# Kernel optimization log

Hardware: AMD Instinct MI355X
Metric: run time of the kernel (lower is better)

## Reference

```python
import jax, jax.numpy as jnp
import numpy as np

N = 100000      # nodes
E = 1600000     # edges (avg degree 16)
NFEAT = 128
NHID = 128
NOUT = 1
BN_EPS = 1e-5


def setup_inputs() -> dict:
    key = jax.random.key(0)
    ks = jax.random.split(key, 8)
    s = 0.05  # weight scale for numerical stability through relu stack
    return {
        "x": jax.random.normal(ks[0], (N, NFEAT), jnp.float32),
        "edge_index": jax.random.randint(ks[1], (2, E), 0, N, dtype=jnp.int64),
        "edge_weight": jax.random.uniform(ks[2], (E,), jnp.float32),
        "conv1_W": jax.random.normal(ks[3], (NFEAT, NHID), jnp.float32) * s,
        "conv1_b": jnp.zeros((NHID,), jnp.float32),
        "conv2_W": jax.random.normal(ks[4], (NHID, NHID), jnp.float32) * s,
        "conv2_b": jnp.zeros((NHID,), jnp.float32),
        "bn1_gamma": jnp.ones((NHID,), jnp.float32),
        "bn1_beta": jnp.zeros((NHID,), jnp.float32),
        "bn2_gamma": jnp.ones((NHID,), jnp.float32),
        "bn2_beta": jnp.zeros((NHID,), jnp.float32),
        "fc1_W": jax.random.normal(ks[5], (NFEAT + 2 * NHID, NHID), jnp.float32) * s,
        "fc1_b": jnp.zeros((NHID,), jnp.float32),
        "fc2_W": jax.random.normal(ks[6], (NHID, NOUT), jnp.float32) * s,
        "fc2_b": jnp.zeros((NOUT,), jnp.float32),
    }


def _gcn_norm(edge_index, edge_weight, num_nodes):
    # PyG gcn_norm: add self-loops (weight 1), symmetric D^-1/2 A D^-1/2.
    row, col = edge_index[0], edge_index[1]
    loop = jnp.arange(num_nodes, dtype=row.dtype)
    rows = jnp.concatenate([row, loop])
    cols = jnp.concatenate([col, loop])
    w = jnp.concatenate([edge_weight, jnp.ones((num_nodes,), edge_weight.dtype)])
    deg = jax.ops.segment_sum(w, cols, num_segments=num_nodes)
    dinv = jnp.where(deg > 0, jax.lax.rsqrt(deg), 0.0)
    norm = dinv[rows] * w * dinv[cols]
    return rows, cols, norm


def _gcn_conv(x, rows, cols, norm, W, b, num_nodes):
    h = x @ W                                  # [N, out]
    msg = h[rows] * norm[:, None]              # gather + scale  [E+N, out]
    out = jax.ops.segment_sum(msg, cols, num_segments=num_nodes)  # scatter-add
    return out + b


def _bn(x, gamma, beta):
    # BatchNorm1d, training-mode batch statistics (biased variance)
    m = jnp.mean(x, axis=0)
    v = jnp.var(x, axis=0)
    return (x - m) * jax.lax.rsqrt(v + BN_EPS) * gamma + beta


def reference(x, edge_index, edge_weight, conv1_W, conv1_b, conv2_W, conv2_b,
              bn1_gamma, bn1_beta, bn2_gamma, bn2_beta,
              fc1_W, fc1_b, fc2_W, fc2_b):
    n = x.shape[0]
    rows, cols, norm = _gcn_norm(edge_index, edge_weight, n)
    h0 = x
    h1 = jax.nn.relu(_gcn_conv(h0, rows, cols, norm, conv1_W, conv1_b, n))
    h1 = _bn(h1, bn1_gamma, bn1_beta)          # dropout p=0 -> identity
    h2 = jax.nn.relu(_gcn_conv(h1, rows, cols, norm, conv2_W, conv2_b, n))
    h2 = _bn(h2, bn2_gamma, bn2_beta)
    cat = jnp.concatenate([h0, h1, h2], axis=1)   # [N, nfeat+2*nhid]
    z = jax.nn.relu(cat @ fc1_W + fc1_b)
    z = jax.nn.relu(z @ fc2_W + fc2_b)
    return z.reshape(-1)
```

## Files before the change

### kernel.cpp

```cpp
#include <hip/hip_runtime.h>

typedef __attribute__((ext_vector_type(8))) short short8;
typedef __attribute__((ext_vector_type(4))) float f32x4;

constexpr int N = 100000;
constexpr int E = 1600000;
constexpr int F = 128;
constexpr float EPS = 1e-5f;
constexpr int NB = (N + 1023) / 1024;

constexpr int R_RNG = 16;
constexpr int BINS = 6250;
constexpr int G2 = 64;
constexpr int NPB = 640;
constexpr int EPB = E / NPB;
constexpr int EPB4 = EPB / 4;

__device__ __forceinline__ short bf16hi(float v) {
  unsigned u = __float_as_uint(v);
  unsigned r = (u + 0x7fffu + ((u >> 16) & 1u)) >> 16;
  return (short)r;
}
__device__ __forceinline__ float bf16f(short h) {
  return __uint_as_float(((unsigned)(unsigned short)h) << 16);
}
__device__ __forceinline__ float bflo(unsigned v) {
  return __uint_as_float(v << 16);
}
__device__ __forceinline__ float bfhi(unsigned v) {
  return __uint_as_float(v & 0xffff0000u);
}

__global__ __launch_bounds__(256) void k_phist(const int* __restrict__ ei, int* __restrict__ Psl) {
  __shared__ int h16[16];
  const int b = blockIdx.x;
  const int tid = threadIdx.x;
  if (tid < 16) h16[tid] = 0;
  __syncthreads();
  const int4* cols4 = (const int4*)(ei + E);
  for (int t = tid; t < EPB4; t += 256) {
    int4 c = cols4[b * EPB4 + t];
    atomicAdd(&h16[c.x / BINS], 1);
    atomicAdd(&h16[c.y / BINS], 1);
    atomicAdd(&h16[c.z / BINS], 1);
    atomicAdd(&h16[c.w / BINS], 1);
  }
  __syncthreads();
  if (tid == 0) {
    int run = 0;
#pragma unroll
    for (int r = 0; r < 16; ++r) { Psl[b * 17 + r] = run; run += h16[r]; }
    Psl[b * 17 + 16] = run;
  }
}

__global__ __launch_bounds__(256) void k_pscatter(const int* __restrict__ ei, const float* __restrict__ ew,
                                                  const int* __restrict__ Psl, int2* __restrict__ pe) {
  __shared__ int cur[16];
  const int b = blockIdx.x;
  const int tid = threadIdx.x;
  if (tid < 16) cur[tid] = Psl[b * 17 + tid];
  __syncthreads();
  const int4* cols4 = (const int4*)(ei + E);
  const int4* rows4 = (const int4*)ei;
  const float4* ew4 = (const float4*)ew;
  const int base = b * EPB;
  for (int t = tid; t < EPB4; t += 256) {
    int4 c = cols4[b * EPB4 + t];
    int4 rr = rows4[b * EPB4 + t];
    float4 w = ew4[b * EPB4 + t];
#pragma unroll
    for (int j = 0; j < 4; ++j) {
      int cc = (j == 0) ? c.x : (j == 1) ? c.y : (j == 2) ? c.z : c.w;
      int rv = (j == 0) ? rr.x : (j == 1) ? rr.y : (j == 2) ? rr.z : rr.w;
      float wv = (j == 0) ? w.x : (j == 1) ? w.y : (j == 2) ? w.z : w.w;
      int r = cc / BINS;
      int pos = base + atomicAdd(&cur[r], 1);
      pe[pos] = make_int2((rv << 13) | (cc - r * BINS), __float_as_int(wv));
    }
  }
}

__global__ __launch_bounds__(256) void k_hist2(const int2* __restrict__ pe, const int* __restrict__ Psl,
                                               int* __restrict__ P) {
  __shared__ int hist[BINS];
  const int r = blockIdx.x / G2;
  const int g = blockIdx.x % G2;
  const int tid = threadIdx.x;
  for (int i = tid; i < BINS; i += 256) hist[i] = 0;
  __syncthreads();
  for (int b = g; b < NPB; b += G2) {
    const int s = Psl[b * 17 + r], e2 = Psl[b * 17 + r + 1];
    const int eb = b * EPB;
    for (int t = s + tid; t < e2; t += 256)
      atomicAdd(&hist[pe[eb + t].x & 0x1FFF], 1);
  }
  __syncthreads();
  for (int i = tid; i < BINS; i += 256) P[(size_t)blockIdx.x * BINS + i] = hist[i];
}

__global__ __launch_bounds__(256) void k_reduce(int* __restrict__ P, int* __restrict__ cnt) {
  int b = blockIdx.x * 256 + threadIdx.x;
  if (b >= N) return;
  int r = b / BINS, lb = b % BINS;
  size_t base = (size_t)r * G2 * BINS + lb;
  int run = 0;
#pragma unroll 4
  for (int g = 0; g < G2; ++g) {
    size_t idx = base + (size_t)g * BINS;
    int v = P[idx];
    P[idx] = run;
    run += v;
  }
  cnt[b] = run;
}

__global__ __launch_bounds__(256) void k_bsum(const int* __restrict__ cnt, int* __restrict__ bsum) {
  __shared__ int sh[256];
  int base = blockIdx.x * 1024 + threadIdx.x * 4;
  int s = 0;
  if (base + 3 < N) {
    int4 v = *(const int4*)&cnt[base];
    s = v.x + v.y + v.z + v.w;
  } else {
#pragma unroll
    for (int j = 0; j < 4; ++j)
      if (base + j < N) s += cnt[base + j];
  }
  sh[threadIdx.x] = s;
  __syncthreads();
  for (int o = 128; o > 0; o >>= 1) {
    if (threadIdx.x < o) sh[threadIdx.x] += sh[threadIdx.x + o];
    __syncthreads();
  }
  if (threadIdx.x == 0) bsum[blockIdx.x] = sh[0];
}

__global__ __launch_bounds__(128) void k_bscan(const int* __restrict__ bsum, int* __restrict__ bbase,
                                               int* __restrict__ offN) {
  __shared__ int sh[128];
  const int t = threadIdx.x;
  int v = (t < NB) ? bsum[t] : 0;
  sh[t] = v;
  __syncthreads();
  for (int o = 1; o < 128; o <<= 1) {
    int u = (t >= o) ? sh[t - o] : 0;
    __syncthreads();
    sh[t] += u;
    __syncthreads();
  }
  if (t < NB) bbase[t] = sh[t] - v;
  if (t == 127) *offN = sh[127];
}

__global__ __launch_bounds__(256) void k_off(const int* __restrict__ cnt, const int* __restrict__ bbase,
                                             int* __restrict__ off) {
  __shared__ int sh[256];
  int base = blockIdx.x * 1024 + threadIdx.x * 4;
  int c[4] = {0, 0, 0, 0};
  if (base + 3 < N) {
    int4 v = *(const int4*)&cnt[base];
    c[0] = v.x; c[1] = v.y; c[2] = v.z; c[3] = v.w;
  } else {
#pragma unroll
    for (int j = 0; j < 4; ++j)
      if (base + j < N) c[j] = cnt[base + j];
  }
  int s = c[0] + c[1] + c[2] + c[3];
  sh[threadIdx.x] = s;
  __syncthreads();
  for (int o = 1; o < 256; o <<= 1) {
    int u = (threadIdx.x >= o) ? sh[threadIdx.x - o] : 0;
    __syncthreads();
    sh[threadIdx.x] += u;
    __syncthreads();
  }
  int run = bbase[blockIdx.x] + sh[threadIdx.x] - s;
#pragma unroll
  for (int j = 0; j < 4; ++j) {
    if (base + j < N) { off[base + j] = run; run += c[j]; }
  }
}

__global__ __launch_bounds__(256) void k_scatter3(const int2* __restrict__ pe, const int* __restrict__ Psl,
                                                  const int* __restrict__ off, const int* __restrict__ P,
                                                  int2* __restrict__ cpair) {
  __shared__ int base[BINS];
  const int r = blockIdx.x / G2;
  const int g = blockIdx.x % G2;
  const int tid = threadIdx.x;
  for (int i = tid; i < BINS; i += 256)
    base[i] = off[r * BINS + i] + P[(size_t)blockIdx.x * BINS + i];
  __syncthreads();
  for (int b = g; b < NPB; b += G2) {
    const int s = Psl[b * 17 + r], e2 = Psl[b * 17 + r + 1];
    const int eb = b * EPB;
    for (int t = s + tid; t < e2; t += 256) {
      int2 p = pe[eb + t];
      int pos = atomicAdd(&base[p.x & 0x1FFF], 1);
      cpair[pos] = make_int2((int)(((unsigned)p.x) >> 13), p.y);
    }
  }
}

__global__ __launch_bounds__(256) void k_degcsc(const int2* __restrict__ cpair, const int* __restrict__ off,
                                                float* __restrict__ dinv) {
  int i = blockIdx.x * 256 + threadIdx.x;
  if (i >= N) return;
  int b = off[i], e2 = off[i + 1];
  float s = 1.0f;
  for (int p = b; p < e2; ++p) s += __int_as_float(cpair[p].y);
  dinv[i] = rsqrtf(s);
}

__global__ __launch_bounds__(256) void k_nrm(const int* __restrict__ off,
                                             const float* __restrict__ dinv, int2* __restrict__ cpair) {
  int i = blockIdx.x * 256 + threadIdx.x;
  if (i >= N) return;
  int b = off[i], e2 = off[i + 1];
  float di = dinv[i];
  for (int p = b; p < e2; ++p) {
    int2 cp = cpair[p];
    cpair[p].y = __float_as_int(dinv[cp.x] * __int_as_float(cp.y) * di);
  }
}

__global__ __launch_bounds__(256) void k_wprep_all(
    const float* __restrict__ W1, const float* __restrict__ W2, const float* __restrict__ Wf1,
    short* __restrict__ wt1h, short* __restrict__ wt1l,
    short* __restrict__ wt2h, short* __restrict__ wt2l,
    short* __restrict__ wtfh, short* __restrict__ wtfl,
    float* __restrict__ st1, float* __restrict__ st2) {
  int idx = blockIdx.x * 256 + threadIdx.x;
  if (idx < 256) st1[idx] = 0.f;
  else if (idx < 512) st2[idx - 256] = 0.f;
  const float* W;
  short *wh, *wl;
  int K, li;
  if (idx < 16384)      { W = W1;  wh = wt1h; wl = wt1l; K = 128; li = idx; }
  else if (idx < 32768) { W = W2;  wh = wt2h; wl = wt2l; K = 128; li = idx - 16384; }
  else if (idx < 81920) { W = Wf1; wh = wtfh; wl = wtfl; K = 384; li = idx - 32768; }
  else return;
  int k = li >> 7, c = li & 127;
  float v = W[(size_t)k * 128 + c];
  short h = bf16hi(v);
  short l = bf16hi(v - bf16f(h));
  wh[(size_t)c * K + k] = h;
  wl[(size_t)c * K + k] = l;
}

__global__ void k_bnparam(const float* __restrict__ st, const float* __restrict__ gamma,
                          const float* __restrict__ beta, float* __restrict__ p) {
  int t = threadIdx.x;
  if (t >= 128) return;
  const float inv_n = 1.0f / (float)N;
  float m = st[t] * inv_n;
  float var = fmaf(-m, m, st[128 + t] * inv_n);
  float sc = gamma[t] * rsqrtf(var + EPS);
  p[t] = sc;
  p[128 + t] = fmaf(-m, sc, beta[t]);
}

template <int KSTEPS, bool OBF16, bool FC2, int AMASK>
__global__ __launch_bounds__(256) void k_gemm_mfma(
    const void* __restrict__ a0, const float* __restrict__ p0,
    const void* __restrict__ a1, const float* __restrict__ p1,
    const void* __restrict__ a2, const float* __restrict__ p2,
    const short* __restrict__ wth, const short* __restrict__ wtl,
    const float* __restrict__ bias, void* __restrict__ Cout,
    const float* __restrict__ wf2, const float* __restrict__ bf2) {
  constexpr int KT = KSTEPS * 32;
  __shared__ short Ah[128][40];
  __shared__ short Al[128][40];
  __shared__ short Bh[128][40];
  __shared__ short Bl[128][40];
  __shared__ float red[2][128];

  const int tid = threadIdx.x;
  const int m0 = blockIdx.x * 128;
  const int sr = tid >> 1;
  const int sk = (tid & 1) * 16;
  const int arow = min(m0 + sr, N - 1);
  const int lane = tid & 63;
  const int lr = lane & 15;
  const int lg = lane >> 4;
  const int wv = tid >> 6;
  const int wr = wv >> 1;
  const int wc = wv & 1;

  f32x4 acc[4][4];
#pragma unroll
  for (int m = 0; m < 4; ++m)
#pragma unroll
    for (int n = 0; n < 4; ++n) acc[m][n] = (f32x4){0.f, 0.f, 0.f, 0.f};

  for (int ks = 0; ks < KSTEPS; ++ks) {
    const int seg = ks >> 2;
    const int koff = (ks & 3) * 32;
    const void* __restrict__ Av = (seg == 0) ? a0 : ((seg == 1) ? a1 : a2);
    const float* __restrict__ P = (seg == 0) ? p0 : ((seg == 1) ? p1 : p2);
    const bool isbf = (AMASK >> seg) & 1;

    float v[16];
    if (isbf) {
      const unsigned short* A16 = (const unsigned short*)Av;
      const uint4* s16 = (const uint4*)&A16[(size_t)arow * F + koff + sk];
      uint4 ua = s16[0], ub = s16[1];
      unsigned uu[8] = {ua.x, ua.y, ua.z, ua.w, ub.x, ub.y, ub.z, ub.w};
#pragma unroll
      for (int j = 0; j < 8; ++j) {
        v[2 * j] = bflo(uu[j]);
        v[2 * j + 1] = bfhi(uu[j]);
      }
    } else {
      const float* A = (const float*)Av;
      const float4* src = (const float4*)(A + (size_t)arow * F + koff + sk);
#pragma unroll
      for (int q = 0; q < 4; ++q) {
        float4 t = src[q];
        v[q * 4 + 0] = t.x; v[q * 4 + 1] = t.y; v[q * 4 + 2] = t.z; v[q * 4 + 3] = t.w;
      }
    }
    if (P) {
      const int c0 = koff + sk;
#pragma unroll
      for (int q = 0; q < 4; ++q) {
        float4 s = *(const float4*)&P[c0 + q * 4];
        float4 b = *(const float4*)&P[128 + c0 + q * 4];
        v[q * 4 + 0] = fmaf(v[q * 4 + 0], s.x, b.x);
        v[q * 4 + 1] = fmaf(v[q * 4 + 1], s.y, b.y);
        v[q * 4 + 2] = fmaf(v[q * 4 + 2], s.z, b.z);
        v[q * 4 + 3] = fmaf(v[q * 4 + 3], s.w, b.w);
      }
    }
    short hh[16], ll[16];
#pragma unroll
    for (int j = 0; j < 16; ++j) {
      hh[j] = bf16hi(v[j]);
      ll[j] = bf16hi(v[j] - bf16f(hh[j]));
    }

    __syncthreads();

    short8 t0, t1, u0, u1;
#pragma unroll
    for (int j = 0; j < 8; ++j) { t0[j] = hh[j]; t1[j] = hh[8 + j]; u0[j] = ll[j]; u1[j] = ll[8 + j]; }
    *(short8*)&Ah[sr][sk] = t0;
    *(short8*)&Ah[sr][sk + 8] = t1;
    *(short8*)&Al[sr][sk] = u0;
    *(short8*)&Al[sr][sk + 8] = u1;

    const size_t wbase = (size_t)sr * KT + ks * 32 + sk;
    *(short8*)&Bh[sr][sk]     = *(const short8*)&wth[wbase];
    *(short8*)&Bh[sr][sk + 8] = *(const short8*)&wth[wbase + 8];
    *(short8*)&Bl[sr][sk]     = *(const short8*)&wtl[wbase];
    *(short8*)&Bl[sr][sk + 8] = *(const short8*)&wtl[wbase + 8];

    __syncthreads();

    short8 afh[4], afl[4], bfh[4], bfl[4];
#pragma unroll
    for (int m = 0; m < 4; ++m) {
      const int r2 = wr * 64 + m * 16 + lr;
      afh[m] = *(const short8*)&Ah[r2][lg * 8];
      afl[m] = *(const short8*)&Al[r2][lg * 8];
    }
#pragma unroll
    for (int n = 0; n < 4; ++n) {
      const int c2 = wc * 64 + n * 16 + lr;
      bfh[n] = *(const short8*)&Bh[c2][lg * 8];
      bfl[n] = *(const short8*)&Bl[c2][lg * 8];
    }
#pragma unroll
    for (int m = 0; m < 4; ++m)
#pragma unroll
      for (int n = 0; n < 4; ++n) {
        acc[m][n] = __builtin_amdgcn_mfma_f32_16x16x32_bf16(afh[m], bfh[n], acc[m][n], 0, 0, 0);
        acc[m][n] = __builtin_amdgcn_mfma_f32_16x16x32_bf16(afl[m], bfh[n], acc[m][n], 0, 0, 0);
        acc[m][n] = __builtin_amdgcn_mfma_f32_16x16x32_bf16(afh[m], bfl[n], acc[m][n], 0, 0, 0);
      }
  }

  float bv[4];
#pragma unroll
  for (int n = 0; n < 4; ++n) bv[n] = bias ? bias[wc * 64 + n * 16 + lr] : 0.f;

  if (FC2) {
    float w2v[4];
#pragma unroll
    for (int n = 0; n < 4; ++n) w2v[n] = wf2[wc * 64 + n * 16 + lr];
#pragma unroll
    for (int m = 0; m < 4; ++m) {
#pragma unroll
      for (int j = 0; j < 4; ++j) {
        float partial = 0.f;
#pragma unroll
        for (int n = 0; n < 4; ++n)
          partial += fmaxf(acc[m][n][j] + bv[n], 0.f) * w2v[n];
#pragma unroll
        for (int o = 8; o >= 1; o >>= 1) partial += __shfl_xor(partial, o, 16);
        if (lr == 0) red[wc][wr * 64 + m * 16 + lg * 4 + j] = partial;
      }
    }
    __syncthreads();
    if (tid < 128) {
      const int row = m0 + tid;
      if (row < N) {
        float s = red[0][tid] + red[1][tid] + bf2[0];
        ((float*)Cout)[row] = fmaxf(s, 0.f);
      }
    }
  } else {
#pragma unroll
    for (int m = 0; m < 4; ++m) {
#pragma unroll
      for (int j = 0; j < 4; ++j) {
        const int row = m0 + wr * 64 + m * 16 + lg * 4 + j;
        if (row < N) {
#pragma unroll
          for (int n = 0; n < 4; ++n) {
            const int col = wc * 64 + n * 16 + lr;
            float o = acc[m][n][j] + bv[n];
            if (bias) o = fmaxf(o, 0.f);
            if (OBF16) {
              ((unsigned short*)Cout)[(size_t)row * F + col] = (unsigned short)bf16hi(o);
            } else {
              ((float*)Cout)[(size_t)row * F + col] = o;
            }
          }
        }
      }
    }
  }
}

__global__ __launch_bounds__(256) void k_agg(
    const unsigned* __restrict__ h,
    const int2* __restrict__ cpair, const int* __restrict__ off,
    const float* __restrict__ dinv, const float* __restrict__ bias,
    unsigned* __restrict__ out) {
  const int i = blockIdx.x * 4 + (threadIdx.x >> 6);
  if (i >= N) return;
  const int lane = threadIdx.x & 63;
  const float di = dinv[i];
  unsigned sv = h[(size_t)i * 64 + lane];
  float acc0 = di * di * bflo(sv);
  float acc1 = di * di * bfhi(sv);
  int e = off[i];
  const int eend = off[i + 1];
  for (; e + 8 <= eend; e += 8) {
    int2 cp[8];
    unsigned vv[8];
#pragma unroll
    for (int j = 0; j < 8; ++j) cp[j] = cpair[e + j];
#pragma unroll
    for (int j = 0; j < 8; ++j) vv[j] = h[(size_t)cp[j].x * 64 + lane];
#pragma unroll
    for (int j = 0; j < 8; ++j) {
      float w = __int_as_float(cp[j].y);
      acc0 = fmaf(w, bflo(vv[j]), acc0);
      acc1 = fmaf(w, bfhi(vv[j]), acc1);
    }
  }
  for (; e < eend; ++e) {
    int2 cp = cpair[e];
    float w = __int_as_float(cp.y);
    unsigned v = h[(size_t)cp.x * 64 + lane];
    acc0 = fmaf(w, bflo(v), acc0);
    acc1 = fmaf(w, bfhi(v), acc1);
  }
  float2 b = *(const float2*)&bias[lane * 2];
  float o0 = fmaxf(acc0 + b.x, 0.f);
  float o1 = fmaxf(acc1 + b.y, 0.f);
  unsigned pack = ((unsigned)(unsigned short)bf16hi(o0)) |
                  (((unsigned)(unsigned short)bf16hi(o1)) << 16);
  out[(size_t)i * 64 + lane] = pack;
}

__global__ __launch_bounds__(256) void k_stats(const unsigned* __restrict__ h2, float* __restrict__ sums) {
  const int cp = threadIdx.x & 63;
  const int q = threadIdx.x >> 6;
  float s0 = 0.f, s1 = 0.f, q0 = 0.f, q1 = 0.f;
  for (int r = blockIdx.x * 4 + q; r < N; r += gridDim.x * 4) {
    unsigned u = h2[(size_t)r * 64 + cp];
    float lo = bflo(u), hi = bfhi(u);
    s0 += lo; s1 += hi;
    q0 = fmaf(lo, lo, q0);
    q1 = fmaf(hi, hi, q1);
  }
  __shared__ float2 sh[256];
  sh[threadIdx.x] = make_float2(s0, s1);
  __syncthreads();
  if (q == 0) {
    float2 a = sh[cp], b = sh[64 + cp], c = sh[128 + cp], d = sh[192 + cp];
    atomicAdd(&sums[2 * cp], a.x + b.x + c.x + d.x);
    atomicAdd(&sums[2 * cp + 1], a.y + b.y + c.y + d.y);
  }
  __syncthreads();
  sh[threadIdx.x] = make_float2(q0, q1);
  __syncthreads();
  if (q == 0) {
    float2 a = sh[cp], b = sh[64 + cp], c = sh[128 + cp], d = sh[192 + cp];
    atomicAdd(&sums[128 + 2 * cp], a.x + b.x + c.x + d.x);
    atomicAdd(&sums[128 + 2 * cp + 1], a.y + b.y + c.y + d.y);
  }
}

extern "C" void kernel_launch(void* const* d_in, const int* in_sizes, int n_in,
                              void* d_out, int out_size, void* d_ws, size_t ws_size,
                              hipStream_t stream) {
  const float* x   = (const float*)d_in[0];
  const int*   ei  = (const int*)d_in[1];
  const float* ew  = (const float*)d_in[2];
  const float* W1  = (const float*)d_in[3];
  const float* b1  = (const float*)d_in[4];
  const float* W2  = (const float*)d_in[5];
  const float* b2  = (const float*)d_in[6];
  const float* g1  = (const float*)d_in[7];
  const float* be1 = (const float*)d_in[8];
  const float* g2  = (const float*)d_in[9];
  const float* be2 = (const float*)d_in[10];
  const float* Wf1 = (const float*)d_in[11];
  const float* bf1 = (const float*)d_in[12];
  const float* Wf2 = (const float*)d_in[13];
  const float* bf2 = (const float*)d_in[14];
  float* out = (float*)d_out;

  char* p = (char*)d_ws;
  auto take = [&](size_t bytes) {
    char* r = p;
    p += (bytes + 255) & ~(size_t)255;
    return r;
  };
  float* st1  = (float*)take(256 * 4);
  float* st2  = (float*)take(256 * 4);
  int*   cnt  = (int*)take((size_t)N * 4);
  int*   off  = (int*)take((size_t)(N + 1) * 4);
  int*   bsum = (int*)take((size_t)NB * 4);
  int*   bbase= (int*)take((size_t)NB * 4);
  int*   Psl  = (int*)take((size_t)NPB * 17 * 4);
  int2*  pe   = (int2*)take((size_t)E * 8);
  int*   Phist= (int*)take((size_t)R_RNG * G2 * BINS * 4);
  float* dinv = (float*)take((size_t)N * 4);
  float* p1   = (float*)take(256 * 4);
  float* p2   = (float*)take(256 * 4);
  short* wt1h = (short*)take((size_t)128 * 128 * 2);
  short* wt1l = (short*)take((size_t)128 * 128 * 2);
  short* wt2h = (short*)take((size_t)128 * 128 * 2);
  short* wt2l = (short*)take((size_t)128 * 128 * 2);
  short* wtfh = (short*)take((size_t)128 * 384 * 2);
  short* wtfl = (short*)take((size_t)128 * 384 * 2);
  int2*  cpair= (int2*)take((size_t)E * 8);
  unsigned short* bufH  = (unsigned short*)take((size_t)N * F * 2);
  unsigned short* bufB16= (unsigned short*)take((size_t)N * F * 2);
  unsigned short* bufC16= (unsigned short*)take((size_t)N * F * 2);

  k_wprep_all<<<320, 256, 0, stream>>>(W1, W2, Wf1, wt1h, wt1l, wt2h, wt2l, wtfh, wtfl, st1, st2);

  k_phist<<<NPB, 256, 0, stream>>>(ei, Psl);
  k_pscatter<<<NPB, 256, 0, stream>>>(ei, ew, Psl, pe);
  k_hist2<<<R_RNG * G2, 256, 0, stream>>>(pe, Psl, Phist);
  k_reduce<<<(N + 255) / 256, 256, 0, stream>>>(Phist, cnt);
  k_bsum<<<NB, 256, 0, stream>>>(cnt, bsum);
  k_bscan<<<1, 128, 0, stream>>>(bsum, bbase, &off[N]);
  k_off<<<NB, 256, 0, stream>>>(cnt, bbase, off);
  k_scatter3<<<R_RNG * G2, 256, 0, stream>>>(pe, Psl, off, Phist, cpair);
  k_degcsc<<<(N + 255) / 256, 256, 0, stream>>>(cpair, off, dinv);
  k_nrm<<<(N + 255) / 256, 256, 0, stream>>>(off, dinv, cpair);

  const int gemm_grid = (N + 127) / 128;
  k_gemm_mfma<4, true, false, 0><<<gemm_grid, 256, 0, stream>>>(
      x, nullptr, nullptr, nullptr, nullptr, nullptr, wt1h, wt1l, nullptr, bufH, nullptr, nullptr);
  k_agg<<<(N + 3) / 4, 256, 0, stream>>>((const unsigned*)bufH, cpair, off, dinv, b1,
                                         (unsigned*)bufB16);
  k_stats<<<256, 256, 0, stream>>>((const unsigned*)bufB16, st1);
  k_bnparam<<<1, 128, 0, stream>>>(st1, g1, be1, p1);
  k_gemm_mfma<4, true, false, 1><<<gemm_grid, 256, 0, stream>>>(
      bufB16, p1, nullptr, nullptr, nullptr, nullptr, wt2h, wt2l, nullptr, bufH, nullptr, nullptr);
  k_agg<<<(N + 3) / 4, 256, 0, stream>>>((const unsigned*)bufH, cpair, off, dinv, b2,
                                         (unsigned*)bufC16);
  k_stats<<<256, 256, 0, stream>>>((const unsigned*)bufC16, st2);
  k_bnparam<<<1, 128, 0, stream>>>(st2, g2, be2, p2);
  k_gemm_mfma<12, false, true, 6><<<gemm_grid, 256, 0, stream>>>(
      x, nullptr, bufB16, p1, bufC16, p2, wtfh, wtfl, bf1, out, Wf2, bf2);
}
```

Measured before the change: 442.3 us.

## Pack edge index and bf16 weight into 32 bits and split aggregation by feature half per XCD

The normalization kernel now writes a compact 4-byte edge record: a 17-bit source index and a 15-bit bf16 weight with the sign bit dropped, valid because weights are non-negative. The aggregation kernel reads these records instead of 8-byte int2 pairs, halving edge-list traffic. Each node is now handled by two blocks, one per 64-column feature half, with block ids mapped so each XCD group works on one half of the features, aiming for better L2 locality of the gathered rows. The costs are bf16 rounding of the edge weights, 2-byte gathers instead of 4-byte ones, and the edge list being read twice per node.

```diff
diff --git a/kernel.cpp b/kernel.cpp
--- a/kernel.cpp
+++ b/kernel.cpp
@@ -214,14 +214,18 @@
 }
 
 __global__ __launch_bounds__(256) void k_nrm(const int* __restrict__ off,
-                                             const float* __restrict__ dinv, int2* __restrict__ cpair) {
+                                             const float* __restrict__ dinv,
+                                             const int2* __restrict__ cpair,
+                                             unsigned* __restrict__ cp4) {
   int i = blockIdx.x * 256 + threadIdx.x;
   if (i >= N) return;
   int b = off[i], e2 = off[i + 1];
   float di = dinv[i];
   for (int p = b; p < e2; ++p) {
     int2 cp = cpair[p];
-    cpair[p].y = __float_as_int(dinv[cp.x] * __int_as_float(cp.y) * di);
+    float w = dinv[cp.x] * __int_as_float(cp.y) * di;
+    unsigned wb = (unsigned)(unsigned short)bf16hi(w);
+    cp4[p] = ((unsigned)cp.x << 15) | (wb & 0x7FFFu);
   }
 }
 
@@ -435,46 +439,40 @@
 }
 
 __global__ __launch_bounds__(256) void k_agg(
-    const unsigned* __restrict__ h,
-    const int2* __restrict__ cpair, const int* __restrict__ off,
+    const unsigned short* __restrict__ h,
+    const unsigned* __restrict__ cp4, const int* __restrict__ off,
     const float* __restrict__ dinv, const float* __restrict__ bias,
-    unsigned* __restrict__ out) {
-  const int i = blockIdx.x * 4 + (threadIdx.x >> 6);
-  if (i >= N) return;
+    unsigned short* __restrict__ out) {
+  const int bid = blockIdx.x;
+  const int xcd = bid & 7;
+  const int half = xcd >> 2;
+  const int i = ((bid >> 3) * 4 + (xcd & 3)) * 4 + (threadIdx.x >> 6);
   const int lane = threadIdx.x & 63;
+  const int co = half * 64 + lane;
   const float di = dinv[i];
-  unsigned sv = h[(size_t)i * 64 + lane];
-  float acc0 = di * di * bflo(sv);
-  float acc1 = di * di * bfhi(sv);
+  float acc = di * di * bf16f((short)h[(size_t)i * F + co]);
   int e = off[i];
   const int eend = off[i + 1];
   for (; e + 8 <= eend; e += 8) {
-    int2 cp[8];
-    unsigned vv[8];
-#pragma unroll
-    for (int j = 0; j < 8; ++j) cp[j] = cpair[e + j];
-#pragma unroll
-    for (int j = 0; j < 8; ++j) vv[j] = h[(size_t)cp[j].x * 64 + lane];
+    unsigned u[8];
+    unsigned short v[8];
+#pragma unroll
+    for (int j = 0; j < 8; ++j) u[j] = cp4[e + j];
+#pragma unroll
+    for (int j = 0; j < 8; ++j) v[j] = h[(size_t)(u[j] >> 15) * F + co];
 #pragma unroll
     for (int j = 0; j < 8; ++j) {
-      float w = __int_as_float(cp[j].y);
-      acc0 = fmaf(w, bflo(vv[j]), acc0);
-      acc1 = fmaf(w, bfhi(vv[j]), acc1);
+      float w = __uint_as_float((u[j] & 0x7FFFu) << 16);
+      acc = fmaf(w, bf16f((short)v[j]), acc);
     }
   }
   for (; e < eend; ++e) {
-    int2 cp = cpair[e];
-    float w = __int_as_float(cp.y);
-    unsigned v = h[(size_t)cp.x * 64 + lane];
-    acc0 = fmaf(w, bflo(v), acc0);
-    acc1 = fmaf(w, bfhi(v), acc1);
-  }
-  float2 b = *(const float2*)&bias[lane * 2];
-  float o0 = fmaxf(acc0 + b.x, 0.f);
-  float o1 = fmaxf(acc1 + b.y, 0.f);
-  unsigned pack = ((unsigned)(unsigned short)bf16hi(o0)) |
-                  (((unsigned)(unsigned short)bf16hi(o1)) << 16);
-  out[(size_t)i * 64 + lane] = pack;
+    unsigned u = cp4[e];
+    float w = __uint_as_float((u & 0x7FFFu) << 16);
+    acc = fmaf(w, bf16f((short)h[(size_t)(u >> 15) * F + co]), acc);
+  }
+  float o = fmaxf(acc + bias[co], 0.f);
+  out[(size_t)i * F + co] = (unsigned short)bf16hi(o);
 }
 
 __global__ __launch_bounds__(256) void k_stats(const unsigned* __restrict__ h2, float* __restrict__ sums) {
@@ -551,6 +549,7 @@
   short* wtfh = (short*)take((size_t)128 * 384 * 2);
   short* wtfl = (short*)take((size_t)128 * 384 * 2);
   int2*  cpair= (int2*)take((size_t)E * 8);
+  unsigned* cp4 = (unsigned*)take((size_t)E * 4);
   unsigned short* bufH  = (unsigned short*)take((size_t)N * F * 2);
   unsigned short* bufB16= (unsigned short*)take((size_t)N * F * 2);
   unsigned short* bufC16= (unsigned short*)take((size_t)N * F * 2);
@@ -566,19 +565,18 @@
   k_off<<<NB, 256, 0, stream>>>(cnt, bbase, off);
   k_scatter3<<<R_RNG * G2, 256, 0, stream>>>(pe, Psl, off, Phist, cpair);
   k_degcsc<<<(N + 255) / 256, 256, 0, stream>>>(cpair, off, dinv);
-  k_nrm<<<(N + 255) / 256, 256, 0, stream>>>(off, dinv, cpair);
+  k_nrm<<<(N + 255) / 256, 256, 0, stream>>>(off, dinv, cpair, cp4);
 
   const int gemm_grid = (N + 127) / 128;
+  const int agg_grid = (N / 4) * 2;
   k_gemm_mfma<4, true, false, 0><<<gemm_grid, 256, 0, stream>>>(
       x, nullptr, nullptr, nullptr, nullptr, nullptr, wt1h, wt1l, nullptr, bufH, nullptr, nullptr);
-  k_agg<<<(N + 3) / 4, 256, 0, stream>>>((const unsigned*)bufH, cpair, off, dinv, b1,
-                                         (unsigned*)bufB16);
+  k_agg<<<agg_grid, 256, 0, stream>>>(bufH, cp4, off, dinv, b1, bufB16);
   k_stats<<<256, 256, 0, stream>>>((const unsigned*)bufB16, st1);
   k_bnparam<<<1, 128, 0, stream>>>(st1, g1, be1, p1);
   k_gemm_mfma<4, true, false, 1><<<gemm_grid, 256, 0, stream>>>(
       bufB16, p1, nullptr, nullptr, nullptr, nullptr, wt2h, wt2l, nullptr, bufH, nullptr, nullptr);
-  k_agg<<<(N + 3) / 4, 256, 0, stream>>>((const unsigned*)bufH, cpair, off, dinv, b2,
-                                         (unsigned*)bufC16);
+  k_agg<<<agg_grid, 256, 0, stream>>>(bufH, cp4, off, dinv, b2, bufC16);
   k_stats<<<256, 256, 0, stream>>>((const unsigned*)bufC16, st2);
   k_bnparam<<<1, 128, 0, stream>>>(st2, g2, be2, p2);
   k_gemm_mfma<12, false, true, 6><<<gemm_grid, 256, 0, stream>>>(
```

New measurement: 530.4 us. 19.9% more time.
